# Kernel optimization log

Measured on AMD Instinct MI355X. Metric: run time of the kernel, lower is better.

## Reference

```python
import jax, jax.numpy as jnp
import numpy as np

N_HEADS = 16
D_MODEL = 1024
D_HEAD = D_MODEL // N_HEADS


def setup_inputs() -> dict:
    key = jax.random.key(0)
    ks = jax.random.split(key, 5)
    scale = 0.02
    x = jax.random.normal(ks[0], (2, 2048, D_MODEL), dtype=jnp.float32)
    # torch.nn.Linear weights: (out_features, in_features)
    w_in = jax.random.normal(ks[1], (3 * D_MODEL, D_MODEL), dtype=jnp.float32) * scale
    b_in = jax.random.normal(ks[2], (3 * D_MODEL,), dtype=jnp.float32) * scale
    w_out = jax.random.normal(ks[3], (D_MODEL, D_MODEL), dtype=jnp.float32) * scale
    b_out = jax.random.normal(ks[4], (D_MODEL,), dtype=jnp.float32) * scale
    return {"x": x, "w_in": w_in, "b_in": b_in, "w_out": w_out, "b_out": b_out}


def reference(x, w_in, b_in, w_out, b_out):
    B, S, D = x.shape
    H, Dh = N_HEADS, D_HEAD
    qkv = x @ w_in.T + b_in                      # [B,S,3D]
    q, k, v = jnp.split(qkv, 3, axis=-1)
    q = q.reshape(B, S, H, Dh).transpose(0, 2, 1, 3)  # [B,H,S,Dh]
    k = k.reshape(B, S, H, Dh).transpose(0, 2, 1, 3)
    v = v.reshape(B, S, H, Dh).transpose(0, 2, 1, 3)
    scores = jnp.einsum('bhqd,bhkd->bhqk', q, k) / jnp.sqrt(jnp.float32(Dh))
    weights = jax.nn.softmax(scores, axis=-1)
    out = jnp.einsum('bhqk,bhkd->bhqd', weights, v)   # [B,H,S,Dh]
    # Faithful to original: reshape WITHOUT transposing heads back
    out = out.reshape(B, S, D)
    return out @ w_out.T + b_out
```

## Files before the change

kernel.cpp:

```cpp
#include <hip/hip_runtime.h>
#include <math.h>

constexpr int D_MODEL = 1024;
constexpr int N_HEADS = 16;
constexpr int D_HEAD  = 64;
constexpr int SEQ     = 2048;
constexpr int BATCH   = 2;
constexpr int M_ROWS  = BATCH * SEQ;
constexpr int QKV_N   = 3 * D_MODEL;
constexpr int KDIM    = 1024;

typedef __bf16 bf16x8 __attribute__((ext_vector_type(8)));
typedef float  f32x4  __attribute__((ext_vector_type(4)));
typedef float  f32x16 __attribute__((ext_vector_type(16)));
typedef unsigned uint2v __attribute__((ext_vector_type(2)));

union U4 { uint4 u; bf16x8 b; ushort s[8]; };

__device__ __forceinline__ unsigned pk2bf(float lo, float hi) {
    union { unsigned u; __bf16 b[2]; } cv;
    cv.b[0] = (__bf16)lo; cv.b[1] = (__bf16)hi;
    return cv.u;
}
__device__ __forceinline__ ushort f2bf(float f) {
    union { ushort s[2]; __bf16 b[2]; } cv;
    cv.b[0] = (__bf16)f;
    return cv.s[0];
}

__device__ __forceinline__ int swz(int row, int bytecol) {
    return row * 128 + (bytecol ^ ((row & 7) << 4));
}

__device__ __forceinline__ void gload16(const void* g, void* l) {
    __builtin_amdgcn_global_load_lds(
        (const __attribute__((address_space(1))) unsigned int*)g,
        (__attribute__((address_space(3))) unsigned int*)l, 16, 0, 0);
}

#define QSCALE 0.18033688011112042f

__global__ __launch_bounds__(256)
void convert3_kernel(const float* __restrict__ x,  ushort* __restrict__ xo,
                     const float* __restrict__ wi, ushort* __restrict__ wio,
                     const float* __restrict__ wo, ushort* __restrict__ woo) {
    const int na = M_ROWS * D_MODEL;
    const int nb = QKV_N * D_MODEL;
    const int nc = D_MODEL * D_MODEL;
    const int total = (na + nb + nc) / 8;
    for (int g = blockIdx.x * blockDim.x + threadIdx.x; g < total;
         g += gridDim.x * blockDim.x) {
        const int i = g * 8;
        const float* src; ushort* dst; int off;
        if (i < na)           { src = x;  dst = xo;  off = i; }
        else if (i < na + nb) { src = wi; dst = wio; off = i - na; }
        else                  { src = wo; dst = woo; off = i - na - nb; }
        const float4 a = *reinterpret_cast<const float4*>(src + off);
        const float4 b = *reinterpret_cast<const float4*>(src + off + 4);
        uint4 o;
        o.x = pk2bf(a.x, a.y); o.y = pk2bf(a.z, a.w);
        o.z = pk2bf(b.x, b.y); o.w = pk2bf(b.z, b.w);
        *reinterpret_cast<uint4*>(dst + off) = o;
    }
}

__device__ __forceinline__ void mfma_gemm_bt_128(
    const ushort* __restrict__ Ag, const ushort* __restrict__ Bg,
    int m0, int n0, ushort* As, ushort* Bs, f32x4 (&acc)[4][4])
{
    const int tid = threadIdx.x;
    const int l   = tid & 63;
    const int rl  = l & 15, hh = l >> 4;
    const int w   = tid >> 6;
    const int wm  = (w >> 1) * 64, wn = (w & 1) * 64;

    const int r0 = tid >> 2;
    const int ce = (tid & 3) * 8;
    const ushort* gA0 = Ag + (size_t)(m0 + r0) * KDIM + ce;
    const ushort* gA1 = gA0 + (size_t)64 * KDIM;
    const ushort* gB0 = Bg + (size_t)(n0 + r0) * KDIM + ce;
    const ushort* gB1 = gB0 + (size_t)64 * KDIM;
    char* lA = (char*)As + tid * 16;
    char* lB = (char*)Bs + tid * 16;

    for (int k0 = 0; k0 < KDIM; k0 += 32) {
        __syncthreads();
        gload16(gA0 + k0, lA);
        gload16(gA1 + k0, lA + 4096);
        gload16(gB0 + k0, lB);
        gload16(gB1 + k0, lB + 4096);
        __syncthreads();

        bf16x8 af[4], bf_[4];
        #pragma unroll
        for (int f = 0; f < 4; ++f)
            af[f]  = *(const bf16x8*)((const char*)As + (wm + f * 16 + rl) * 64 + hh * 16);
        #pragma unroll
        for (int f = 0; f < 4; ++f)
            bf_[f] = *(const bf16x8*)((const char*)Bs + (wn + f * 16 + rl) * 64 + hh * 16);
        #pragma unroll
        for (int i = 0; i < 4; ++i)
            #pragma unroll
            for (int j = 0; j < 4; ++j)
                acc[i][j] = __builtin_amdgcn_mfma_f32_16x16x32_bf16(af[i], bf_[j], acc[i][j], 0, 0, 0);
    }
}

__global__ __launch_bounds__(256)
void qkv_mfma_kernel(const ushort* __restrict__ xb, const ushort* __restrict__ wb,
                     const float* __restrict__ b_in,
                     ushort* __restrict__ Q, ushort* __restrict__ K, ushort* __restrict__ V) {
    __shared__ __align__(16) ushort As[128 * 32];
    __shared__ __align__(16) ushort Bs[128 * 32];

    f32x4 acc[4][4];
    #pragma unroll
    for (int i = 0; i < 4; ++i)
        #pragma unroll
        for (int j = 0; j < 4; ++j) acc[i][j] = (f32x4){0.f, 0.f, 0.f, 0.f};

    const int m0 = blockIdx.y * 128, n0 = blockIdx.x * 128;
    mfma_gemm_bt_128(xb, wb, m0, n0, As, Bs, acc);

    const int l  = threadIdx.x & 63, w = threadIdx.x >> 6;
    const int rl = l & 15, hh = l >> 4;
    const int mb = m0 + (w >> 1) * 64, nb = n0 + (w & 1) * 64;

    #pragma unroll
    for (int j = 0; j < 4; ++j) {
        const int n  = nb + j * 16 + rl;
        const float bias = b_in[n];
        const int t  = n >> 10;
        const int jj = n & 1023;
        const int h  = jj >> 6;
        const int d  = jj & 63;
        ushort* dst = (t == 0) ? Q : (t == 1) ? K : V;
        const float sc = (t == 0) ? QSCALE : 1.0f;
        #pragma unroll
        for (int i = 0; i < 4; ++i)
            #pragma unroll
            for (int r = 0; r < 4; ++r) {
                const int m = mb + i * 16 + hh * 4 + r;
                const int b = m >> 11;
                const int s = m & (SEQ - 1);
                dst[((size_t)(b * N_HEADS + h) * SEQ + s) * D_HEAD + d] =
                    f2bf((acc[i][j][r] + bias) * sc);
            }
    }
}

__global__ __launch_bounds__(256)
void attn_mfma_kernel(const ushort* __restrict__ Q, const ushort* __restrict__ K,
                      const ushort* __restrict__ V, ushort* __restrict__ A) {
    __shared__ __align__(16) char Ks[2][64 * 128];
    __shared__ __align__(16) char Vs[2][64 * 128];

    const int tid = threadIdx.x;
    const int w   = tid >> 6;
    const int l   = tid & 63;
    const int l31 = l & 31;
    const int lh  = l >> 5;

    const int bid = blockIdx.x;
    const int nid = (bid & 7) * 64 + (bid >> 3);
    const int bh  = nid >> 4;
    const int qt  = nid & 15;

    const size_t base = (size_t)bh * SEQ * D_HEAD;
    const int qbase = qt * 128 + w * 32;

    bf16x8 qf[4];
    {
        const ushort* qp = Q + base + (size_t)(qbase + l31) * D_HEAD + lh * 8;
        #pragma unroll
        for (int c = 0; c < 4; ++c) {
            U4 t; t.u = *(const uint4*)(qp + c * 16);
            qf[c] = t.b;
        }
    }

    f32x16 ot0, ot1;
    #pragma unroll
    for (int r = 0; r < 16; ++r) { ot0[r] = 0.f; ot1[r] = 0.f; }
    float m_run = -INFINITY, l_run = 0.0f;

    const int sr  = tid >> 2, seg = tid & 3;
    const int kp  = (tid & 31) * 2, db = tid >> 5;
    const ushort* gK  = K + base + (size_t)sr * D_HEAD + seg * 8;
    const ushort* gV0 = V + base + (size_t)kp * D_HEAD + db * 8;
    const ushort* gV1 = gV0 + D_HEAD;

    uint4 ka, kb; U4 va, vb;
    ka   = *(const uint4*)(gK);
    kb   = *(const uint4*)(gK + 32);
    va.u = *(const uint4*)(gV0);
    vb.u = *(const uint4*)(gV1);
    {
        char* kd = Ks[0]; char* vd = Vs[0];
        *(uint4*)(kd + swz(sr, seg * 16))      = ka;
        *(uint4*)(kd + swz(sr, seg * 16 + 64)) = kb;
        #pragma unroll
        for (int i = 0; i < 8; ++i) {
            const int d = db * 8 + i;
            *(unsigned*)(vd + d * 128 + ((kp * 2) ^ ((d & 7) << 4))) =
                (unsigned)va.s[i] | ((unsigned)vb.s[i] << 16);
        }
    }

    constexpr int NT = SEQ / 64;
    for (int t = 0; t < NT; ++t) {
        const int cur = t & 1;
        __syncthreads();

        if (t + 1 < NT) {
            const size_t off = (size_t)(t + 1) * 64 * D_HEAD;
            ka   = *(const uint4*)(gK + off);
            kb   = *(const uint4*)(gK + off + 32);
            va.u = *(const uint4*)(gV0 + off);
            vb.u = *(const uint4*)(gV1 + off);
        }
        const char* kbuf = Ks[cur];
        const char* vbuf = Vs[cur];

        f32x16 st0, st1;
        #pragma unroll
        for (int r = 0; r < 16; ++r) { st0[r] = 0.f; st1[r] = 0.f; }
        #pragma unroll
        for (int c = 0; c < 4; ++c) {
            const bf16x8 kf0 = *(const bf16x8*)(kbuf + swz(l31,      c * 32 + lh * 16));
            st0 = __builtin_amdgcn_mfma_f32_32x32x16_bf16(kf0, qf[c], st0, 0, 0, 0);
            const bf16x8 kf1 = *(const bf16x8*)(kbuf + swz(32 + l31, c * 32 + lh * 16));
            st1 = __builtin_amdgcn_mfma_f32_32x32x16_bf16(kf1, qf[c], st1, 0, 0, 0);
        }

        float mx[16];
        #pragma unroll
        for (int r = 0; r < 16; ++r) mx[r] = fmaxf(st0[r], st1[r]);
        #pragma unroll
        for (int s = 8; s > 0; s >>= 1)
            #pragma unroll
            for (int r = 0; r < s; ++r) mx[r] = fmaxf(mx[r], mx[r + s]);
        float tm = fmaxf(mx[0], __shfl_xor(mx[0], 32, 64));

        if (!__all(tm <= m_run + 8.0f)) {
            const float mnew = fmaxf(m_run, tm);
            const float corr = __builtin_amdgcn_exp2f(m_run - mnew);
            l_run *= corr;
            #pragma unroll
            for (int r = 0; r < 16; ++r) { ot0[r] *= corr; ot1[r] *= corr; }
            m_run = mnew;
        }
        float ps0 = 0.f, ps1 = 0.f;
        #pragma unroll
        for (int r = 0; r < 16; ++r) {
            st0[r] = __builtin_amdgcn_exp2f(st0[r] - m_run); ps0 += st0[r];
            st1[r] = __builtin_amdgcn_exp2f(st1[r] - m_run); ps1 += st1[r];
        }
        float ps = ps0 + ps1;
        ps += __shfl_xor(ps, 32, 64);
        l_run += ps;

        bf16x8 paf[4];
        #pragma unroll
        for (int t32 = 0; t32 < 2; ++t32) {
            const f32x16& s = t32 ? st1 : st0;
            const unsigned q0 = pk2bf(s[0],  s[1]);
            const unsigned q1 = pk2bf(s[2],  s[3]);
            const unsigned q2 = pk2bf(s[4],  s[5]);
            const unsigned q3 = pk2bf(s[6],  s[7]);
            const unsigned q4 = pk2bf(s[8],  s[9]);
            const unsigned q5 = pk2bf(s[10], s[11]);
            const unsigned q6 = pk2bf(s[12], s[13]);
            const unsigned q7 = pk2bf(s[14], s[15]);
            const uint2v x = __builtin_amdgcn_permlane32_swap(q0, q2, false, false);
            const uint2v y = __builtin_amdgcn_permlane32_swap(q1, q3, false, false);
            const uint2v z = __builtin_amdgcn_permlane32_swap(q4, q6, false, false);
            const uint2v u = __builtin_amdgcn_permlane32_swap(q5, q7, false, false);
            U4 f0; f0.u.x = x[0]; f0.u.y = y[0]; f0.u.z = x[1]; f0.u.w = y[1];
            U4 f1; f1.u.x = z[0]; f1.u.y = u[0]; f1.u.z = z[1]; f1.u.w = u[1];
            paf[t32 * 2]     = f0.b;
            paf[t32 * 2 + 1] = f1.b;
        }

        #pragma unroll
        for (int kc = 0; kc < 4; ++kc) {
            const bf16x8 vf0 = *(const bf16x8*)(vbuf + swz(l31,      kc * 32 + lh * 16));
            ot0 = __builtin_amdgcn_mfma_f32_32x32x16_bf16(vf0, paf[kc], ot0, 0, 0, 0);
            const bf16x8 vf1 = *(const bf16x8*)(vbuf + swz(32 + l31, kc * 32 + lh * 16));
            ot1 = __builtin_amdgcn_mfma_f32_32x32x16_bf16(vf1, paf[kc], ot1, 0, 0, 0);
        }

        if (t + 1 < NT) {
            char* kd = Ks[cur ^ 1]; char* vd = Vs[cur ^ 1];
            *(uint4*)(kd + swz(sr, seg * 16))      = ka;
            *(uint4*)(kd + swz(sr, seg * 16 + 64)) = kb;
            #pragma unroll
            for (int i = 0; i < 8; ++i) {
                const int d = db * 8 + i;
                *(unsigned*)(vd + d * 128 + ((kp * 2) ^ ((d & 7) << 4))) =
                    (unsigned)va.s[i] | ((unsigned)vb.s[i] << 16);
            }
        }
    }

    const float inv = 1.0f / l_run;
    ushort* ap = A + base + (size_t)(qbase + l31) * D_HEAD;
    #pragma unroll
    for (int dt = 0; dt < 2; ++dt) {
        const f32x16& o = dt ? ot1 : ot0;
        #pragma unroll
        for (int g = 0; g < 4; ++g) {
            const int d0 = dt * 32 + g * 8 + lh * 4;
            uint2 s2;
            s2.x = pk2bf(o[g * 4 + 0] * inv, o[g * 4 + 1] * inv);
            s2.y = pk2bf(o[g * 4 + 2] * inv, o[g * 4 + 3] * inv);
            *(uint2*)(ap + d0) = s2;
        }
    }
}

__global__ __launch_bounds__(256)
void out_mfma_kernel(const ushort* __restrict__ Ab, const ushort* __restrict__ wb,
                     const float* __restrict__ b_out, float* __restrict__ out) {
    __shared__ __align__(16) ushort As[128 * 32];
    __shared__ __align__(16) ushort Bs[128 * 32];

    f32x4 acc[4][4];
    #pragma unroll
    for (int i = 0; i < 4; ++i)
        #pragma unroll
        for (int j = 0; j < 4; ++j) acc[i][j] = (f32x4){0.f, 0.f, 0.f, 0.f};

    const int m0 = blockIdx.y * 128, n0 = blockIdx.x * 128;
    mfma_gemm_bt_128(Ab, wb, m0, n0, As, Bs, acc);

    const int l  = threadIdx.x & 63, w = threadIdx.x >> 6;
    const int rl = l & 15, hh = l >> 4;
    const int mb = m0 + (w >> 1) * 64, nb = n0 + (w & 1) * 64;

    #pragma unroll
    for (int j = 0; j < 4; ++j) {
        const int n = nb + j * 16 + rl;
        const float bias = b_out[n];
        #pragma unroll
        for (int i = 0; i < 4; ++i)
            #pragma unroll
            for (int r = 0; r < 4; ++r) {
                const int m = mb + i * 16 + hh * 4 + r;
                out[(size_t)m * D_MODEL + n] = acc[i][j][r] + bias;
            }
    }
}

extern "C" void kernel_launch(void* const* d_in, const int* in_sizes, int n_in,
                              void* d_out, int out_size, void* d_ws, size_t ws_size,
                              hipStream_t stream) {
    const float* x     = (const float*)d_in[0];
    const float* w_in  = (const float*)d_in[1];
    const float* b_in  = (const float*)d_in[2];
    const float* w_out = (const float*)d_in[3];
    const float* b_out = (const float*)d_in[4];
    float* out = (float*)d_out;

    const size_t T = (size_t)BATCH * N_HEADS * SEQ * D_HEAD;
    ushort* Qw  = (ushort*)d_ws;
    ushort* Kw  = Qw + T;
    ushort* Vw  = Kw + T;
    ushort* Aw  = Vw + T;
    ushort* xb  = Aw + T;
    ushort* wib = xb + (size_t)M_ROWS * D_MODEL;
    ushort* wob = wib + (size_t)QKV_N * D_MODEL;

    convert3_kernel<<<2048, 256, 0, stream>>>(x, xb, w_in, wib, w_out, wob);

    qkv_mfma_kernel<<<dim3(QKV_N / 128, M_ROWS / 128), 256, 0, stream>>>(
        xb, wib, b_in, Qw, Kw, Vw);
    attn_mfma_kernel<<<512, 256, 0, stream>>>(Qw, Kw, Vw, Aw);
    out_mfma_kernel<<<dim3(D_MODEL / 128, M_ROWS / 128), 256, 0, stream>>>(
        Aw, wob, b_out, out);
}
```

Baseline: 127.5 us.

## Split attention KV range in two halves with separate combine kernel

```diff
diff --git a/kernel.cpp b/kernel.cpp
--- a/kernel.cpp
+++ b/kernel.cpp
@@ -9,6 +9,7 @@
 constexpr int M_ROWS  = BATCH * SEQ;
 constexpr int QKV_N   = 3 * D_MODEL;
 constexpr int KDIM    = 1024;
+constexpr int NROWS   = BATCH * N_HEADS * SEQ;
 
 typedef __bf16 bf16x8 __attribute__((ext_vector_type(8)));
 typedef float  f32x4  __attribute__((ext_vector_type(4)));
@@ -150,8 +151,9 @@
 }
 
 __global__ __launch_bounds__(256)
-void attn_mfma_kernel(const ushort* __restrict__ Q, const ushort* __restrict__ K,
-                      const ushort* __restrict__ V, ushort* __restrict__ A) {
+void attn_mfma_split_kernel(const ushort* __restrict__ Q, const ushort* __restrict__ K,
+                            const ushort* __restrict__ V, ushort* __restrict__ Op,
+                            float2* __restrict__ ml) {
     __shared__ __align__(16) char Ks[2][64 * 128];
     __shared__ __align__(16) char Vs[2][64 * 128];
 
@@ -161,12 +163,15 @@
     const int l31 = l & 31;
     const int lh  = l >> 5;
 
-    const int bid = blockIdx.x;
-    const int nid = (bid & 7) * 64 + (bid >> 3);
-    const int bh  = nid >> 4;
-    const int qt  = nid & 15;
-
-    const size_t base = (size_t)bh * SEQ * D_HEAD;
+    const int bid  = blockIdx.x;
+    const int nid  = (bid & 7) * 128 + (bid >> 3);
+    const int bh   = nid >> 5;
+    const int rem  = nid & 31;
+    const int half = rem >> 4;
+    const int qt   = rem & 15;
+
+    const size_t base  = (size_t)bh * SEQ * D_HEAD;
+    const size_t kbase = base + (size_t)half * 1024 * D_HEAD;
     const int qbase = qt * 128 + w * 32;
 
     bf16x8 qf[4];
@@ -186,8 +191,8 @@
 
     const int sr  = tid >> 2, seg = tid & 3;
     const int kp  = (tid & 31) * 2, db = tid >> 5;
-    const ushort* gK  = K + base + (size_t)sr * D_HEAD + seg * 8;
-    const ushort* gV0 = V + base + (size_t)kp * D_HEAD + db * 8;
+    const ushort* gK  = K + kbase + (size_t)sr * D_HEAD + seg * 8;
+    const ushort* gV0 = V + kbase + (size_t)kp * D_HEAD + db * 8;
     const ushort* gV1 = gV0 + D_HEAD;
 
     uint4 ka, kb; U4 va, vb;
@@ -207,7 +212,7 @@
         }
     }
 
-    constexpr int NT = SEQ / 64;
+    constexpr int NT = 1024 / 64;
     for (int t = 0; t < NT; ++t) {
         const int cur = t & 1;
         __syncthreads();
@@ -303,8 +308,8 @@
         }
     }
 
-    const float inv = 1.0f / l_run;
-    ushort* ap = A + base + (size_t)(qbase + l31) * D_HEAD;
+    const size_t grow = (size_t)bh * SEQ + qbase + l31;
+    ushort* op = Op + ((size_t)half * NROWS + grow) * D_HEAD;
     #pragma unroll
     for (int dt = 0; dt < 2; ++dt) {
         const f32x16& o = dt ? ot1 : ot0;
@@ -312,11 +317,38 @@
         for (int g = 0; g < 4; ++g) {
             const int d0 = dt * 32 + g * 8 + lh * 4;
             uint2 s2;
-            s2.x = pk2bf(o[g * 4 + 0] * inv, o[g * 4 + 1] * inv);
-            s2.y = pk2bf(o[g * 4 + 2] * inv, o[g * 4 + 3] * inv);
-            *(uint2*)(ap + d0) = s2;
-        }
-    }
+            s2.x = pk2bf(o[g * 4 + 0], o[g * 4 + 1]);
+            s2.y = pk2bf(o[g * 4 + 2], o[g * 4 + 3]);
+            *(uint2*)(op + d0) = s2;
+        }
+    }
+    if (lh == 0) ml[(size_t)half * NROWS + grow] = make_float2(m_run, l_run);
+}
+
+__global__ __launch_bounds__(256)
+void combine_kernel(const ushort* __restrict__ Op, const float2* __restrict__ ml,
+                    ushort* __restrict__ A) {
+    const int idx = blockIdx.x * 256 + threadIdx.x;
+    const int row = idx >> 3;
+    const int dc  = (idx & 7) * 8;
+    const float2 a = ml[row];
+    const float2 b = ml[NROWS + row];
+    const float m  = fmaxf(a.x, b.x);
+    float w1 = __builtin_amdgcn_exp2f(a.x - m);
+    float w2 = __builtin_amdgcn_exp2f(b.x - m);
+    const float inv = 1.0f / (w1 * a.y + w2 * b.y);
+    w1 *= inv; w2 *= inv;
+    U4 o1, o2;
+    o1.u = *(const uint4*)(Op + (size_t)row * D_HEAD + dc);
+    o2.u = *(const uint4*)(Op + ((size_t)NROWS + row) * D_HEAD + dc);
+    uint4 r;
+    float v[8];
+    #pragma unroll
+    for (int i = 0; i < 8; ++i)
+        v[i] = w1 * (float)o1.b[i] + w2 * (float)o2.b[i];
+    r.x = pk2bf(v[0], v[1]); r.y = pk2bf(v[2], v[3]);
+    r.z = pk2bf(v[4], v[5]); r.w = pk2bf(v[6], v[7]);
+    *(uint4*)(A + (size_t)row * D_HEAD + dc) = r;
 }
 
 __global__ __launch_bounds__(256)
@@ -366,16 +398,19 @@
     ushort* Qw  = (ushort*)d_ws;
     ushort* Kw  = Qw + T;
     ushort* Vw  = Kw + T;
-    ushort* Aw  = Vw + T;
-    ushort* xb  = Aw + T;
-    ushort* wib = xb + (size_t)M_ROWS * D_MODEL;
+    ushort* Opw = Vw + T;
+    ushort* xb  = Opw + T;
+    ushort* wib = xb + T;
     ushort* wob = wib + (size_t)QKV_N * D_MODEL;
+    float2* mlw = (float2*)(wob + (size_t)D_MODEL * D_MODEL);
+    ushort* Aw  = Qw;
 
     convert3_kernel<<<2048, 256, 0, stream>>>(x, xb, w_in, wib, w_out, wob);
 
     qkv_mfma_kernel<<<dim3(QKV_N / 128, M_ROWS / 128), 256, 0, stream>>>(
         xb, wib, b_in, Qw, Kw, Vw);
-    attn_mfma_kernel<<<512, 256, 0, stream>>>(Qw, Kw, Vw, Aw);
+    attn_mfma_split_kernel<<<1024, 256, 0, stream>>>(Qw, Kw, Vw, Opw, mlw);
+    combine_kernel<<<NROWS * 8 / 256, 256, 0, stream>>>(Opw, mlw, Aw);
     out_mfma_kernel<<<dim3(D_MODEL / 128, M_ROWS / 128), 256, 0, stream>>>(
         Aw, wob, b_out, out);
 }
```

Result: slower. 134.3 us (+5.3%).
